# Kernel optimization log

Measured on AMD Instinct MI355X. Metric: run time of the kernel, lower is better.

## Reference

```python
import jax, jax.numpy as jnp
import numpy as np

N, NNODES, CIN, COUT = 64, 512, 32, 64


def setup_inputs() -> dict:
    key = jax.random.key(0)
    k1, k2, k3, k4, k5 = jax.random.split(key, 5)
    A = jax.random.normal(k1, (N, NNODES, NNODES), dtype=jnp.float32)
    X = jax.random.normal(k2, (N, NNODES, CIN), dtype=jnp.float32)
    A_coeffs = jax.random.normal(k3, (5 + 2 * CIN,), dtype=jnp.float32)
    x_num = 4 + 2 * CIN
    scale = np.sqrt(2.0) / (COUT + x_num)
    X_coeffs_1 = jax.random.normal(k4, (COUT, x_num), dtype=jnp.float32) * scale
    X_coeffs_2 = jax.random.normal(k5, (COUT, x_num), dtype=jnp.float32) * scale
    return {"A": A, "X": X, "A_coeffs": A_coeffs,
            "X_coeffs_1": X_coeffs_1, "X_coeffs_2": X_coeffs_2}


def _forward(A, X, A_coeffs, W1, W2):
    n = A.shape[-1]
    C = X.shape[-1]
    Xt = jnp.swapaxes(X, -1, -2)                      # N,C,n
    diag = jnp.diagonal(A, axis1=-2, axis2=-1)        # N,n
    mean_diag = diag.mean(-1)                         # N
    mean_cols = A.mean(-1)                            # N,n
    mean_all = mean_cols.mean(-1)                     # N
    mean_X = Xt.mean(-1)                              # N,C

    c = A_coeffs
    w6 = c[5:5 + C]                                   # coeffs for a6 (X_i + X_j)
    w7 = c[5 + C:5 + 2 * C]                           # coeffs for a7 (mean_X)
    # Fold the 'd,ndij->nij' contraction over the 7 basis tensors into
    # scalar/row/col broadcast terms (identical math, no N x (5+2C) x n x n tensor).
    s = jnp.einsum('c,nci->ni', w6, Xt)               # N,n
    const = c[1] * mean_all + c[2] * mean_diag + jnp.einsum('c,nc->n', w7, mean_X)
    vec = c[3] * mean_cols + c[4] * diag + s          # N,n
    A_t = c[0] * A + const[:, None, None] + vec[:, :, None] + vec[:, None, :]

    # X basis out_x: N x (4+2C) x n, order [x1, x2, x3, x4, x5, x6]
    ones_n = jnp.ones((1, 1, n), A.dtype)
    out_x = jnp.concatenate([
        Xt,                                           # x1: N,C,n
        mean_X[:, :, None] * ones_n,                  # x2: N,C,n
        mean_cols[:, None, :],                        # x3: N,1,n
        diag[:, None, :],                             # x4: N,1,n
        mean_diag[:, None, None] * ones_n,            # x5: N,1,n
        mean_all[:, None, None] * ones_n,             # x6: N,1,n
    ], axis=1)
    X1 = jnp.einsum('bd,ndi->nbi', W1, out_x)         # N,B,n
    X2 = jnp.einsum('bd,ndi->nbi', W2, out_x)         # N,B,n
    out = jnp.einsum('nij,nbj->nbi', A_t, X1) / n + X2  # N,B,n
    return jnp.swapaxes(out, -1, -2)                  # N,n,B


def reference(A, X, A_coeffs, X_coeffs_1, X_coeffs_2):
    return _forward(A, X, A_coeffs, X_coeffs_1, X_coeffs_2)
```

## Files before the change

### kernel.cpp

```cpp
#include <hip/hip_runtime.h>
#include <hip/hip_bf16.h>

#define NB 64
#define NN 512
#define CI 32
#define CO 64
#define XN 68
#define YR 80

typedef __attribute__((ext_vector_type(8))) short bf16x8;
typedef __attribute__((ext_vector_type(4))) float f32x4;

__device__ inline short f2bf(float f) {
  union { __hip_bfloat16 h; unsigned short u; } cv;
  cv.h = __float2bfloat16(f);
  return (short)cv.u;
}

__device__ inline bf16x8 cvt8(float4 a, float4 b) {
  bf16x8 r;
  r[0] = f2bf(a.x); r[1] = f2bf(a.y); r[2] = f2bf(a.z); r[3] = f2bf(a.w);
  r[4] = f2bf(b.x); r[5] = f2bf(b.y); r[6] = f2bf(b.z); r[7] = f2bf(b.w);
  return r;
}

__device__ inline bf16x8 cvt8s(float4 a, float4 b, float s) {
  bf16x8 r;
  r[0] = f2bf(a.x * s); r[1] = f2bf(a.y * s); r[2] = f2bf(a.z * s); r[3] = f2bf(a.w * s);
  r[4] = f2bf(b.x * s); r[5] = f2bf(b.y * s); r[6] = f2bf(b.z * s); r[7] = f2bf(b.w * s);
  return r;
}

__global__ __launch_bounds__(256) void k1x(
    const float* __restrict__ A, const float* __restrict__ X,
    const float* __restrict__ cf, const float* __restrict__ W1,
    float* __restrict__ mc, float* __restrict__ dg, float* __restrict__ vec,
    float* __restrict__ pA, float* __restrict__ pD,
    float* __restrict__ pmX, float* __restrict__ ptC, float* __restrict__ pS,
    unsigned short* __restrict__ Yext) {
  int b = blockIdx.x, ch = blockIdx.y;
  int t = threadIdx.x, w = t >> 6, lane = t & 63;
  int r0 = ch * 16;
  const float* Ab = A + (size_t)b * NN * NN;
  __shared__ float sXc[16][33];
  __shared__ float scf[69];
  __shared__ float sMc[16], sDg[16], sVec[16], wsum[4];

  if (t < 69) scf[t] = cf[t];
  {
    int j = t >> 4, c = (t & 15) * 2;
    float2 xv = *(const float2*)(X + ((size_t)b * NN + r0 + j) * CI + c);
    sXc[j][c] = xv.x; sXc[j][c + 1] = xv.y;
  }
  float4 v0[4], v1[4];
#pragma unroll
  for (int m = 0; m < 4; ++m) {
    const float* rp = Ab + (size_t)(r0 + w * 4 + m) * NN;
    v0[m] = *(const float4*)(rp + lane * 4);
    v1[m] = *(const float4*)(rp + 256 + lane * 4);
  }
  float accR = 0.f;
#pragma unroll
  for (int m = 0; m < 4; ++m) {
    float s = (v0[m].x + v0[m].y) + (v0[m].z + v0[m].w) +
              (v1[m].x + v1[m].y) + (v1[m].z + v1[m].w);
#pragma unroll
    for (int off = 1; off < 64; off <<= 1) s += __shfl_xor(s, off, 64);
    if (lane == 0) {
      float m_ = s * (1.0f / NN);
      mc[b * NN + r0 + w * 4 + m] = m_;
      sMc[w * 4 + m] = m_;
    }
    accR += s;
  }
  if (lane == 0) wsum[w] = accR;
  if (t < 16) {
    float d = Ab[(size_t)(r0 + t) * NN + r0 + t];
    dg[b * NN + r0 + t] = d;
    sDg[t] = d;
  }
  __syncthreads();

  if (t < 16) {
    float u = 0.f;
#pragma unroll
    for (int c = 0; c < CI; ++c) u += scf[5 + c] * sXc[t][c];
    float vj = scf[3] * sMc[t] + scf[4] * sDg[t] + u;
    vec[b * NN + r0 + t] = vj;
    sVec[t] = vj;
  } else if (t == 16) {
    pA[b * 32 + ch] = wsum[0] + wsum[1] + wsum[2] + wsum[3];
    float sd = 0.f;
#pragma unroll
    for (int k = 0; k < 16; ++k) sd += sDg[k];
    pD[b * 32 + ch] = sd;
  }

  {
    int ra = lane & 15, kg = lane >> 4, g = lane >> 4;
    const float* wp = W1 + (w * 16 + ra) * XN + kg * 8;
    bf16x8 wf = cvt8(*(const float4*)wp, *(const float4*)(wp + 4));
    const float* xp = &sXc[ra][kg * 8];
    bf16x8 xf = cvt8(*(const float4*)xp, *(const float4*)(xp + 4));
    f32x4 zero = {0.f, 0.f, 0.f, 0.f};
    f32x4 d = __builtin_amdgcn_mfma_f32_16x16x32_bf16(xf, wf, zero, 0, 0, 0);
    union { unsigned short u[4]; uint2 v; } pk;
#pragma unroll
    for (int r = 0; r < 4; ++r) pk.u[r] = (unsigned short)f2bf(d[r]);
    *(uint2*)(Yext + ((size_t)b * YR + w * 16 + ra) * NN + r0 + g * 4) = pk.v;
  }
  if (t < 16) {
    Yext[((size_t)b * YR + 64) * NN + r0 + t] = (unsigned short)f2bf(sMc[t]);
  } else if (t < 32) {
    Yext[((size_t)b * YR + 65) * NN + r0 + (t - 16)] = (unsigned short)f2bf(sDg[t - 16]);
  } else if (t < 32 + 224) {
    int u2 = t - 32;
    int row = 66 + (u2 >> 4), col = r0 + (u2 & 15);
    Yext[((size_t)b * YR + row) * NN + col] = 0;
  }
  __syncthreads();

  if (t < 32) {
    float s1 = 0.f, s2 = 0.f;
#pragma unroll
    for (int r = 0; r < 16; ++r) {
      float xv = sXc[r][t];
      s1 += xv;
      s2 += sVec[r] * xv;
    }
    pmX[((size_t)b * 32 + ch) * 32 + t] = s1;
    ptC[((size_t)b * 32 + ch) * 32 + t] = s2;
  } else if (t < 35) {
    float s = 0.f;
    if (t == 32) { for (int r = 0; r < 16; ++r) s += sVec[r]; }
    if (t == 33) { for (int r = 0; r < 16; ++r) s += sVec[r] * sMc[r]; }
    if (t == 34) { for (int r = 0; r < 16; ++r) s += sVec[r] * sDg[r]; }
    pS[((size_t)b * 32 + ch) * 3 + (t - 32)] = s;
  }
}

__global__ __launch_bounds__(256) void kW(
    const float* __restrict__ cf, const float* __restrict__ W1,
    const float* __restrict__ W2, const float* __restrict__ pA,
    const float* __restrict__ pD, const float* __restrict__ pmX,
    const float* __restrict__ ptC, const float* __restrict__ pS,
    float* __restrict__ colv, float* __restrict__ sconst) {
  int gb = blockIdx.x, t = threadIdx.x;
  int bb0 = gb * 4;
  __shared__ float sW1[64][69], sW2[64][69];
  __shared__ float mXs[4][33], tCs[4][33];
  __shared__ float scal[4][6];
  __shared__ float scf[69];
  if (t < 69) scf[t] = cf[t];
  for (int idx = t; idx < 64 * XN; idx += 256) {
    int r = idx / XN, c = idx - r * XN;
    sW1[r][c] = W1[idx];
    sW2[r][c] = W2[idx];
  }
  if (t < 128) {
    int bb = t >> 5, c = t & 31, b = bb0 + bb;
    float s1 = 0.f, s2 = 0.f;
#pragma unroll
    for (int k = 0; k < 32; ++k) {
      s1 += pmX[((size_t)b * 32 + k) * 32 + c];
      s2 += ptC[((size_t)b * 32 + k) * 32 + c];
    }
    mXs[bb][c] = s1 * (1.0f / NN);
    tCs[bb][c] = s2;
  } else if (t < 132) {
    int bb = t - 128, b = bb0 + bb;
    float sA = 0.f, sD = 0.f;
#pragma unroll
    for (int k = 0; k < 32; ++k) { sA += pA[b * 32 + k]; sD += pD[b * 32 + k]; }
    scal[bb][0] = sD * (1.0f / NN);
    scal[bb][1] = sA * (1.0f / ((float)NN * (float)NN));
  } else if (t < 136) {
    int bb = t - 132, b = bb0 + bb;
    float s1 = 0.f, s2 = 0.f, s3 = 0.f;
#pragma unroll
    for (int k = 0; k < 32; ++k) {
      s1 += pS[((size_t)b * 32 + k) * 3 + 0];
      s2 += pS[((size_t)b * 32 + k) * 3 + 1];
      s3 += pS[((size_t)b * 32 + k) * 3 + 2];
    }
    scal[bb][2] = s1; scal[bb][3] = s2; scal[bb][4] = s3;
  }
  __syncthreads();
  if (t < 4) {
    float s7 = 0.f;
#pragma unroll
    for (int c = 0; c < CI; ++c) s7 += scf[5 + CI + c] * mXs[t][c];
    sconst[bb0 + t] = scf[1] * scal[t][1] + scf[2] * scal[t][0] + s7;
  }
  {
    int bb = t >> 6, o = t & 63, b = bb0 + bb;
    float w1mX = 0.f, a1 = 0.f, a2 = 0.f, wt = 0.f;
#pragma unroll
    for (int c = 0; c < CI; ++c) {
      float m = mXs[bb][c];
      w1mX += sW1[o][c] * m;
      a1 += sW1[o][CI + c] * m;
      a2 += sW2[o][CI + c] * m;
      wt += sW1[o][c] * tCs[bb][c];
    }
    float smd = scal[bb][0], sma = scal[bb][1];
    a1 += sW1[o][66] * smd + sW1[o][67] * sma;
    a2 += sW2[o][66] * smd + sW2[o][67] * sma;
    float we0 = sW1[o][64], we1 = sW1[o][65];
    float S1n = w1mX + a1 + we0 * sma + we1 * smd;
    float SVn = (wt + a1 * scal[bb][2] + we0 * scal[bb][3] + we1 * scal[bb][4]) * (1.0f / NN);
    float4 cva = make_float4(S1n, a2 + SVn, sW2[o][64] + scf[0] * a1, sW2[o][65]);
    float4 cvb = make_float4(we0, we1, 0.f, 0.f);
    *(float4*)&colv[((size_t)b * CO + o) * 8] = cva;
    *(float4*)&colv[((size_t)b * CO + o) * 8 + 4] = cvb;
  }
}

__global__ __launch_bounds__(256) void k5_mfma(
    const float* __restrict__ A, const unsigned short* __restrict__ Yext,
    const float* __restrict__ X, const float* __restrict__ W2,
    const float* __restrict__ vec, const float* __restrict__ mc,
    const float* __restrict__ dg, const float* __restrict__ colv,
    const float* __restrict__ sconst, const float* __restrict__ cf,
    float* __restrict__ out) {
  int b = blockIdx.x, ic = blockIdx.y;
  int t = threadIdx.x, w = t >> 6, lane = t & 63;
  int ra = lane & 15, kg = lane >> 4, g = lane >> 4;
  int i0 = ic * 64 + w * 16;

  float c0n = cf[0] * (1.0f / NN);
  const float* Arow = A + ((size_t)(b * NN + i0 + ra)) * NN;
  const unsigned short* Yb = Yext + (size_t)b * YR * NN;

  f32x4 acc[4] = {{0.f, 0.f, 0.f, 0.f}, {0.f, 0.f, 0.f, 0.f},
                  {0.f, 0.f, 0.f, 0.f}, {0.f, 0.f, 0.f, 0.f}};
  f32x4 acc4 = {0.f, 0.f, 0.f, 0.f};

#pragma unroll
  for (int jt = 0; jt < 16; ++jt) {
    int kb = jt * 32 + kg * 8;
    float4 a0 = *(const float4*)(Arow + kb);
    float4 a1 = *(const float4*)(Arow + kb + 4);
    bf16x8 af = cvt8s(a0, a1, c0n);
#pragma unroll
    for (int to = 0; to < 4; ++to) {
      bf16x8 bf = *(const bf16x8*)(Yb + (size_t)(to * 16 + ra) * NN + kb);
      acc[to] = __builtin_amdgcn_mfma_f32_16x16x32_bf16(af, bf, acc[to], 0, 0, 0);
    }
    bf16x8 bf4 = *(const bf16x8*)(Yb + (size_t)(64 + ra) * NN + kb);
    acc4 = __builtin_amdgcn_mfma_f32_16x16x32_bf16(af, bf4, acc4, 0, 0, 0);
  }

  {
    const float* xp = X + (size_t)(b * NN + i0 + ra) * CI + kg * 8;
    bf16x8 xf = cvt8(*(const float4*)xp, *(const float4*)(xp + 4));
#pragma unroll
    for (int to = 0; to < 4; ++to) {
      const float* wp = W2 + (size_t)(to * 16 + ra) * XN + kg * 8;
      bf16x8 wf = cvt8(*(const float4*)wp, *(const float4*)(wp + 4));
      acc[to] = __builtin_amdgcn_mfma_f32_16x16x32_bf16(xf, wf, acc[to], 0, 0, 0);
    }
  }

  float Gm[4], Gd[4];
#pragma unroll
  for (int r = 0; r < 4; ++r) {
    Gm[r] = __shfl(acc4[r], lane & 48, 64);
    Gd[r] = __shfl(acc4[r], (lane & 48) | 1, 64);
  }

  float4 v4 = *(const float4*)&vec[b * NN + i0 + g * 4];
  float4 m4 = *(const float4*)&mc[b * NN + i0 + g * 4];
  float4 d4 = *(const float4*)&dg[b * NN + i0 + g * 4];
  float sc = sconst[b];
  float vp[4] = {v4.x + sc, v4.y + sc, v4.z + sc, v4.w + sc};
  float mr[4] = {m4.x, m4.y, m4.z, m4.w};
  float dr[4] = {d4.x, d4.y, d4.z, d4.w};

#pragma unroll
  for (int to = 0; to < 4; ++to) {
    int o = to * 16 + ra;
    float4 cva = *(const float4*)&colv[((size_t)b * CO + o) * 8];
    float4 cvb = *(const float4*)&colv[((size_t)b * CO + o) * 8 + 4];
#pragma unroll
    for (int r = 0; r < 4; ++r) {
      float val = acc[to][r] + vp[r] * cva.x + cva.y + mr[r] * cva.z +
                  dr[r] * cva.w + Gm[r] * cvb.x + Gd[r] * cvb.y;
      out[((size_t)(b * NN + i0 + g * 4 + r)) * CO + o] = val;
    }
  }
}

extern "C" void kernel_launch(void* const* d_in, const int* in_sizes, int n_in,
                              void* d_out, int out_size, void* d_ws, size_t ws_size,
                              hipStream_t stream) {
  const float* A = (const float*)d_in[0];
  const float* X = (const float*)d_in[1];
  const float* cf = (const float*)d_in[2];
  const float* W1 = (const float*)d_in[3];
  const float* W2 = (const float*)d_in[4];
  float* out = (float*)d_out;

  float* p = (float*)d_ws;
  float* mc = p;      p += NB * NN;
  float* dg = p;      p += NB * NN;
  float* vec = p;     p += NB * NN;
  float* pA = p;      p += NB * 32;
  float* pD = p;      p += NB * 32;
  float* pmX = p;     p += NB * 32 * 32;
  float* ptC = p;     p += NB * 32 * 32;
  float* pS = p;      p += NB * 32 * 3;
  float* colv = p;    p += NB * CO * 8;
  float* sconst = p;  p += NB;
  unsigned short* Yext = (unsigned short*)p;

  k1x<<<dim3(NB, 32), 256, 0, stream>>>(A, X, cf, W1, mc, dg, vec,
                                        pA, pD, pmX, ptC, pS, Yext);
  kW<<<16, 256, 0, stream>>>(cf, W1, W2, pA, pD, pmX, ptC, pS, colv, sconst);
  k5_mfma<<<dim3(NB, 8), 256, 0, stream>>>(A, Yext, X, W2, vec, mc, dg,
                                           colv, sconst, cf, out);
}
```

Before: 54.59 us.

## Split k5 reduction across two waves per row group and prescale Y by c0/n

The main A·Y MFMA kernel now uses 512 threads, with two waves splitting the 512-wide K dimension for each 16-row group. Partial accumulators are summed through shared memory before the epilogue. The c0/n scale moves from per-element A conversion in k5 into the Y rows written by k1x, so k5 no longer multiplies every A element. This doubles the waves in flight to hide global-load latency, at the cost of a shared-memory reduction, a barrier, and idle waves during the epilogue. Because the scale is now applied to Y before the bf16 rounding rather than to A, rounding behaviour changes slightly.

```diff
diff --git a/kernel.cpp b/kernel.cpp
--- a/kernel.cpp
+++ b/kernel.cpp
@@ -21,13 +21,6 @@
   bf16x8 r;
   r[0] = f2bf(a.x); r[1] = f2bf(a.y); r[2] = f2bf(a.z); r[3] = f2bf(a.w);
   r[4] = f2bf(b.x); r[5] = f2bf(b.y); r[6] = f2bf(b.z); r[7] = f2bf(b.w);
-  return r;
-}
-
-__device__ inline bf16x8 cvt8s(float4 a, float4 b, float s) {
-  bf16x8 r;
-  r[0] = f2bf(a.x * s); r[1] = f2bf(a.y * s); r[2] = f2bf(a.z * s); r[3] = f2bf(a.w * s);
-  r[4] = f2bf(b.x * s); r[5] = f2bf(b.y * s); r[6] = f2bf(b.z * s); r[7] = f2bf(b.w * s);
   return r;
 }
 
@@ -81,6 +74,8 @@
   }
   __syncthreads();
 
+  float c0n = scf[0] * (1.0f / NN);
+
   if (t < 16) {
     float u = 0.f;
 #pragma unroll
@@ -106,13 +101,13 @@
     f32x4 d = __builtin_amdgcn_mfma_f32_16x16x32_bf16(xf, wf, zero, 0, 0, 0);
     union { unsigned short u[4]; uint2 v; } pk;
 #pragma unroll
-    for (int r = 0; r < 4; ++r) pk.u[r] = (unsigned short)f2bf(d[r]);
+    for (int r = 0; r < 4; ++r) pk.u[r] = (unsigned short)f2bf(d[r] * c0n);
     *(uint2*)(Yext + ((size_t)b * YR + w * 16 + ra) * NN + r0 + g * 4) = pk.v;
   }
   if (t < 16) {
-    Yext[((size_t)b * YR + 64) * NN + r0 + t] = (unsigned short)f2bf(sMc[t]);
+    Yext[((size_t)b * YR + 64) * NN + r0 + t] = (unsigned short)f2bf(sMc[t] * c0n);
   } else if (t < 32) {
-    Yext[((size_t)b * YR + 65) * NN + r0 + (t - 16)] = (unsigned short)f2bf(sDg[t - 16]);
+    Yext[((size_t)b * YR + 65) * NN + r0 + (t - 16)] = (unsigned short)f2bf(sDg[t - 16] * c0n);
   } else if (t < 32 + 224) {
     int u2 = t - 32;
     int row = 66 + (u2 >> 4), col = r0 + (u2 & 15);
@@ -216,19 +211,20 @@
   }
 }
 
-__global__ __launch_bounds__(256) void k5_mfma(
+__global__ __launch_bounds__(512, 4) void k5_mfma(
     const float* __restrict__ A, const unsigned short* __restrict__ Yext,
     const float* __restrict__ X, const float* __restrict__ W2,
     const float* __restrict__ vec, const float* __restrict__ mc,
     const float* __restrict__ dg, const float* __restrict__ colv,
-    const float* __restrict__ sconst, const float* __restrict__ cf,
-    float* __restrict__ out) {
+    const float* __restrict__ sconst, float* __restrict__ out) {
   int b = blockIdx.x, ic = blockIdx.y;
   int t = threadIdx.x, w = t >> 6, lane = t & 63;
+  int rg = w >> 1, q = w & 1;
   int ra = lane & 15, kg = lane >> 4, g = lane >> 4;
-  int i0 = ic * 64 + w * 16;
-
-  float c0n = cf[0] * (1.0f / NN);
+  int i0 = ic * 64 + rg * 16;
+  __shared__ float sAcc[4][16][68];
+  __shared__ float sG4[4][16][2];
+
   const float* Arow = A + ((size_t)(b * NN + i0 + ra)) * NN;
   const unsigned short* Yb = Yext + (size_t)b * YR * NN;
 
@@ -237,11 +233,11 @@
   f32x4 acc4 = {0.f, 0.f, 0.f, 0.f};
 
 #pragma unroll
-  for (int jt = 0; jt < 16; ++jt) {
-    int kb = jt * 32 + kg * 8;
+  for (int jt = 0; jt < 8; ++jt) {
+    int kb = q * 256 + jt * 32 + kg * 8;
     float4 a0 = *(const float4*)(Arow + kb);
     float4 a1 = *(const float4*)(Arow + kb + 4);
-    bf16x8 af = cvt8s(a0, a1, c0n);
+    bf16x8 af = cvt8(a0, a1);
 #pragma unroll
     for (int to = 0; to < 4; ++to) {
       bf16x8 bf = *(const bf16x8*)(Yb + (size_t)(to * 16 + ra) * NN + kb);
@@ -251,42 +247,75 @@
     acc4 = __builtin_amdgcn_mfma_f32_16x16x32_bf16(af, bf4, acc4, 0, 0, 0);
   }
 
-  {
-    const float* xp = X + (size_t)(b * NN + i0 + ra) * CI + kg * 8;
-    bf16x8 xf = cvt8(*(const float4*)xp, *(const float4*)(xp + 4));
+  float4 v4, m4, d4;
+  float sc = 0.f;
+  float4 cva[4], cvb[4];
+  if (q == 1) {
+#pragma unroll
+    for (int to = 0; to < 4; ++to)
+#pragma unroll
+      for (int r = 0; r < 4; ++r)
+        sAcc[rg][g * 4 + r][to * 16 + ra] = acc[to][r];
+    if (ra < 2) {
+#pragma unroll
+      for (int r = 0; r < 4; ++r) sG4[rg][g * 4 + r][ra] = acc4[r];
+    }
+  } else {
+    v4 = *(const float4*)&vec[b * NN + i0 + g * 4];
+    m4 = *(const float4*)&mc[b * NN + i0 + g * 4];
+    d4 = *(const float4*)&dg[b * NN + i0 + g * 4];
+    sc = sconst[b];
 #pragma unroll
     for (int to = 0; to < 4; ++to) {
-      const float* wp = W2 + (size_t)(to * 16 + ra) * XN + kg * 8;
-      bf16x8 wf = cvt8(*(const float4*)wp, *(const float4*)(wp + 4));
-      acc[to] = __builtin_amdgcn_mfma_f32_16x16x32_bf16(xf, wf, acc[to], 0, 0, 0);
-    }
-  }
-
-  float Gm[4], Gd[4];
-#pragma unroll
-  for (int r = 0; r < 4; ++r) {
-    Gm[r] = __shfl(acc4[r], lane & 48, 64);
-    Gd[r] = __shfl(acc4[r], (lane & 48) | 1, 64);
-  }
-
-  float4 v4 = *(const float4*)&vec[b * NN + i0 + g * 4];
-  float4 m4 = *(const float4*)&mc[b * NN + i0 + g * 4];
-  float4 d4 = *(const float4*)&dg[b * NN + i0 + g * 4];
-  float sc = sconst[b];
-  float vp[4] = {v4.x + sc, v4.y + sc, v4.z + sc, v4.w + sc};
-  float mr[4] = {m4.x, m4.y, m4.z, m4.w};
-  float dr[4] = {d4.x, d4.y, d4.z, d4.w};
-
-#pragma unroll
-  for (int to = 0; to < 4; ++to) {
-    int o = to * 16 + ra;
-    float4 cva = *(const float4*)&colv[((size_t)b * CO + o) * 8];
-    float4 cvb = *(const float4*)&colv[((size_t)b * CO + o) * 8 + 4];
+      int o = to * 16 + ra;
+      cva[to] = *(const float4*)&colv[((size_t)b * CO + o) * 8];
+      cvb[to] = *(const float4*)&colv[((size_t)b * CO + o) * 8 + 4];
+    }
+  }
+  __syncthreads();
+
+  if (q == 0) {
+#pragma unroll
+    for (int to = 0; to < 4; ++to)
+#pragma unroll
+      for (int r = 0; r < 4; ++r)
+        acc[to][r] += sAcc[rg][g * 4 + r][to * 16 + ra];
+    if (ra < 2) {
+#pragma unroll
+      for (int r = 0; r < 4; ++r) acc4[r] += sG4[rg][g * 4 + r][ra];
+    }
+
+    {
+      const float* xp = X + (size_t)(b * NN + i0 + ra) * CI + kg * 8;
+      bf16x8 xf = cvt8(*(const float4*)xp, *(const float4*)(xp + 4));
+#pragma unroll
+      for (int to = 0; to < 4; ++to) {
+        const float* wp = W2 + (size_t)(to * 16 + ra) * XN + kg * 8;
+        bf16x8 wf = cvt8(*(const float4*)wp, *(const float4*)(wp + 4));
+        acc[to] = __builtin_amdgcn_mfma_f32_16x16x32_bf16(xf, wf, acc[to], 0, 0, 0);
+      }
+    }
+
+    float Gm[4], Gd[4];
 #pragma unroll
     for (int r = 0; r < 4; ++r) {
-      float val = acc[to][r] + vp[r] * cva.x + cva.y + mr[r] * cva.z +
-                  dr[r] * cva.w + Gm[r] * cvb.x + Gd[r] * cvb.y;
-      out[((size_t)(b * NN + i0 + g * 4 + r)) * CO + o] = val;
+      Gm[r] = __shfl(acc4[r], lane & 48, 64);
+      Gd[r] = __shfl(acc4[r], (lane & 48) | 1, 64);
+    }
+
+    float vp[4] = {v4.x + sc, v4.y + sc, v4.z + sc, v4.w + sc};
+    float mr[4] = {m4.x, m4.y, m4.z, m4.w};
+    float dr[4] = {d4.x, d4.y, d4.z, d4.w};
+
+#pragma unroll
+    for (int to = 0; to < 4; ++to) {
+      int o = to * 16 + ra;
+#pragma unroll
+      for (int r = 0; r < 4; ++r) {
+        float val = acc[to][r] + vp[r] * cva[to].x + cva[to].y + mr[r] * cva[to].z +
+                    dr[r] * cva[to].w + Gm[r] * cvb[to].x + Gd[r] * cvb[to].y;
+        out[((size_t)(b * NN + i0 + g * 4 + r)) * CO + o] = val;
+      }
     }
   }
 }
@@ -317,6 +346,6 @@
   k1x<<<dim3(NB, 32), 256, 0, stream>>>(A, X, cf, W1, mc, dg, vec,
                                         pA, pD, pmX, ptC, pS, Yext);
   kW<<<16, 256, 0, stream>>>(cf, W1, W2, pA, pD, pmX, ptC, pS, colv, sconst);
-  k5_mfma<<<dim3(NB, 8), 256, 0, stream>>>(A, Yext, X, W2, vec, mc, dg,
-                                           colv, sconst, cf, out);
-}
+  k5_mfma<<<dim3(NB, 8), 512, 0, stream>>>(A, Yext, X, W2, vec, mc, dg,
+                                           colv, sconst, out);
+}
```

After: 56.09 us. +2.8%, slower.

## Stage A tiles through double-buffered swizzled LDS and split output columns across waves

Applied to the files above, without the earlier changes.

The main GEMM kernel now uses 512-thread blocks. Each block cooperatively loads 64x64 chunks of A, converts them to bf16 and stores them in double-buffered, XOR-swizzled shared memory, prefetching the next chunk while MFMAs run on the current one. Waves are split into row-group and output-column halves, and the Gm/Gd extras are exchanged through shared memory instead of shuffles. The c0/n scale is folded into Y when k1x writes it, so A no longer needs a per-element multiply, and the grid is reordered so consecutive blocks share a batch. The cost is more block-level synchronisation and more shared memory per block.

```diff
diff --git a/kernel.cpp b/kernel.cpp
--- a/kernel.cpp
+++ b/kernel.cpp
@@ -21,13 +21,6 @@
   bf16x8 r;
   r[0] = f2bf(a.x); r[1] = f2bf(a.y); r[2] = f2bf(a.z); r[3] = f2bf(a.w);
   r[4] = f2bf(b.x); r[5] = f2bf(b.y); r[6] = f2bf(b.z); r[7] = f2bf(b.w);
-  return r;
-}
-
-__device__ inline bf16x8 cvt8s(float4 a, float4 b, float s) {
-  bf16x8 r;
-  r[0] = f2bf(a.x * s); r[1] = f2bf(a.y * s); r[2] = f2bf(a.z * s); r[3] = f2bf(a.w * s);
-  r[4] = f2bf(b.x * s); r[5] = f2bf(b.y * s); r[6] = f2bf(b.z * s); r[7] = f2bf(b.w * s);
   return r;
 }
 
@@ -81,6 +74,8 @@
   }
   __syncthreads();
 
+  float c0n = scf[0] * (1.0f / NN);
+
   if (t < 16) {
     float u = 0.f;
 #pragma unroll
@@ -106,13 +101,13 @@
     f32x4 d = __builtin_amdgcn_mfma_f32_16x16x32_bf16(xf, wf, zero, 0, 0, 0);
     union { unsigned short u[4]; uint2 v; } pk;
 #pragma unroll
-    for (int r = 0; r < 4; ++r) pk.u[r] = (unsigned short)f2bf(d[r]);
+    for (int r = 0; r < 4; ++r) pk.u[r] = (unsigned short)f2bf(d[r] * c0n);
     *(uint2*)(Yext + ((size_t)b * YR + w * 16 + ra) * NN + r0 + g * 4) = pk.v;
   }
   if (t < 16) {
-    Yext[((size_t)b * YR + 64) * NN + r0 + t] = (unsigned short)f2bf(sMc[t]);
+    Yext[((size_t)b * YR + 64) * NN + r0 + t] = (unsigned short)f2bf(sMc[t] * c0n);
   } else if (t < 32) {
-    Yext[((size_t)b * YR + 65) * NN + r0 + (t - 16)] = (unsigned short)f2bf(sDg[t - 16]);
+    Yext[((size_t)b * YR + 65) * NN + r0 + (t - 16)] = (unsigned short)f2bf(sDg[t - 16] * c0n);
   } else if (t < 32 + 224) {
     int u2 = t - 32;
     int row = 66 + (u2 >> 4), col = r0 + (u2 & 15);
@@ -216,77 +211,112 @@
   }
 }
 
-__global__ __launch_bounds__(256) void k5_mfma(
+__global__ __launch_bounds__(512, 4) void k5_mfma(
     const float* __restrict__ A, const unsigned short* __restrict__ Yext,
     const float* __restrict__ X, const float* __restrict__ W2,
     const float* __restrict__ vec, const float* __restrict__ mc,
     const float* __restrict__ dg, const float* __restrict__ colv,
-    const float* __restrict__ sconst, const float* __restrict__ cf,
-    float* __restrict__ out) {
-  int b = blockIdx.x, ic = blockIdx.y;
+    const float* __restrict__ sconst, float* __restrict__ out) {
+  int ic = blockIdx.x, b = blockIdx.y;
   int t = threadIdx.x, w = t >> 6, lane = t & 63;
+  int rg = w >> 1, oc = w & 1;
   int ra = lane & 15, kg = lane >> 4, g = lane >> 4;
-  int i0 = ic * 64 + w * 16;
-
-  float c0n = cf[0] * (1.0f / NN);
-  const float* Arow = A + ((size_t)(b * NN + i0 + ra)) * NN;
+  int i0 = ic * 64;
+  int wr0 = rg * 16;
+  __shared__ unsigned short sA[2][64 * 64];
+  __shared__ float sGm[64], sGd[64];
+
   const unsigned short* Yb = Yext + (size_t)b * YR * NN;
 
-  f32x4 acc[4] = {{0.f, 0.f, 0.f, 0.f}, {0.f, 0.f, 0.f, 0.f},
-                  {0.f, 0.f, 0.f, 0.f}, {0.f, 0.f, 0.f, 0.f}};
+  int st_r = t >> 3, st_k = t & 7;
+  const float* Agl = A + ((size_t)(b * NN + i0 + st_r)) * NN + st_k * 8;
+  int st_addr = st_r * 64 + ((st_k ^ (st_r & 7)) << 3);
+
+  {
+    float4 a0 = *(const float4*)(Agl);
+    float4 a1 = *(const float4*)(Agl + 4);
+    *(bf16x8*)&sA[0][st_addr] = cvt8(a0, a1);
+  }
+  __syncthreads();
+
+  f32x4 acc[2] = {{0.f, 0.f, 0.f, 0.f}, {0.f, 0.f, 0.f, 0.f}};
   f32x4 acc4 = {0.f, 0.f, 0.f, 0.f};
-
-#pragma unroll
-  for (int jt = 0; jt < 16; ++jt) {
-    int kb = jt * 32 + kg * 8;
-    float4 a0 = *(const float4*)(Arow + kb);
-    float4 a1 = *(const float4*)(Arow + kb + 4);
-    bf16x8 af = cvt8s(a0, a1, c0n);
-#pragma unroll
-    for (int to = 0; to < 4; ++to) {
-      bf16x8 bf = *(const bf16x8*)(Yb + (size_t)(to * 16 + ra) * NN + kb);
-      acc[to] = __builtin_amdgcn_mfma_f32_16x16x32_bf16(af, bf, acc[to], 0, 0, 0);
-    }
-    bf16x8 bf4 = *(const bf16x8*)(Yb + (size_t)(64 + ra) * NN + kb);
-    acc4 = __builtin_amdgcn_mfma_f32_16x16x32_bf16(af, bf4, acc4, 0, 0, 0);
-  }
-
-  {
-    const float* xp = X + (size_t)(b * NN + i0 + ra) * CI + kg * 8;
+  int arow = wr0 + ra;
+  int abase = arow * 64;
+  int aswz = arow & 7;
+
+  for (int c = 0; c < 8; ++c) {
+    int cur = c & 1;
+    float4 na0, na1;
+    if (c < 7) {
+      na0 = *(const float4*)(Agl + (c + 1) * 64);
+      na1 = *(const float4*)(Agl + (c + 1) * 64 + 4);
+    }
+#pragma unroll
+    for (int kb = 0; kb < 2; ++kb) {
+      bf16x8 af = *(const bf16x8*)&sA[cur][abase + (((kb * 4 + kg) ^ aswz) << 3)];
+      int kcol = c * 64 + kb * 32 + kg * 8;
+#pragma unroll
+      for (int to = 0; to < 2; ++to) {
+        bf16x8 bf = *(const bf16x8*)(Yb + (size_t)(oc * 32 + to * 16 + ra) * NN + kcol);
+        acc[to] = __builtin_amdgcn_mfma_f32_16x16x32_bf16(af, bf, acc[to], 0, 0, 0);
+      }
+      if (oc == 0) {
+        bf16x8 bf4 = *(const bf16x8*)(Yb + (size_t)(64 + ra) * NN + kcol);
+        acc4 = __builtin_amdgcn_mfma_f32_16x16x32_bf16(af, bf4, acc4, 0, 0, 0);
+      }
+    }
+    if (c < 7) {
+      *(bf16x8*)&sA[cur ^ 1][st_addr] = cvt8(na0, na1);
+    }
+    __syncthreads();
+  }
+
+  {
+    const float* xp = X + (size_t)(b * NN + i0 + wr0 + ra) * CI + kg * 8;
     bf16x8 xf = cvt8(*(const float4*)xp, *(const float4*)(xp + 4));
 #pragma unroll
-    for (int to = 0; to < 4; ++to) {
-      const float* wp = W2 + (size_t)(to * 16 + ra) * XN + kg * 8;
+    for (int to = 0; to < 2; ++to) {
+      const float* wp = W2 + (size_t)(oc * 32 + to * 16 + ra) * XN + kg * 8;
       bf16x8 wf = cvt8(*(const float4*)wp, *(const float4*)(wp + 4));
       acc[to] = __builtin_amdgcn_mfma_f32_16x16x32_bf16(xf, wf, acc[to], 0, 0, 0);
     }
   }
 
-  float Gm[4], Gd[4];
-#pragma unroll
-  for (int r = 0; r < 4; ++r) {
-    Gm[r] = __shfl(acc4[r], lane & 48, 64);
-    Gd[r] = __shfl(acc4[r], (lane & 48) | 1, 64);
-  }
-
-  float4 v4 = *(const float4*)&vec[b * NN + i0 + g * 4];
-  float4 m4 = *(const float4*)&mc[b * NN + i0 + g * 4];
-  float4 d4 = *(const float4*)&dg[b * NN + i0 + g * 4];
+  if (oc == 0 && ra < 2) {
+#pragma unroll
+    for (int r = 0; r < 4; ++r) {
+      if (ra == 0) sGm[wr0 + g * 4 + r] = acc4[r];
+      else         sGd[wr0 + g * 4 + r] = acc4[r];
+    }
+  }
+  __syncthreads();
+
+  float4 v4 = *(const float4*)&vec[b * NN + i0 + wr0 + g * 4];
+  float4 m4 = *(const float4*)&mc[b * NN + i0 + wr0 + g * 4];
+  float4 d4 = *(const float4*)&dg[b * NN + i0 + wr0 + g * 4];
   float sc = sconst[b];
   float vp[4] = {v4.x + sc, v4.y + sc, v4.z + sc, v4.w + sc};
   float mr[4] = {m4.x, m4.y, m4.z, m4.w};
   float dr[4] = {d4.x, d4.y, d4.z, d4.w};
-
-#pragma unroll
-  for (int to = 0; to < 4; ++to) {
-    int o = to * 16 + ra;
+  float Gm[4], Gd[4];
+#pragma unroll
+  for (int r = 0; r < 4; ++r) {
+    int row = wr0 + g * 4 + r;
+    Gm[r] = sGm[row];
+    Gd[r] = sGd[row];
+  }
+
+#pragma unroll
+  for (int to = 0; to < 2; ++to) {
+    int o = oc * 32 + to * 16 + ra;
     float4 cva = *(const float4*)&colv[((size_t)b * CO + o) * 8];
     float4 cvb = *(const float4*)&colv[((size_t)b * CO + o) * 8 + 4];
 #pragma unroll
     for (int r = 0; r < 4; ++r) {
       float val = acc[to][r] + vp[r] * cva.x + cva.y + mr[r] * cva.z +
                   dr[r] * cva.w + Gm[r] * cvb.x + Gd[r] * cvb.y;
-      out[((size_t)(b * NN + i0 + g * 4 + r)) * CO + o] = val;
+      out[((size_t)(b * NN + i0 + wr0 + g * 4 + r)) * CO + o] = val;
     }
   }
 }
@@ -317,6 +347,6 @@
   k1x<<<dim3(NB, 32), 256, 0, stream>>>(A, X, cf, W1, mc, dg, vec,
                                         pA, pD, pmX, ptC, pS, Yext);
   kW<<<16, 256, 0, stream>>>(cf, W1, W2, pA, pD, pmX, ptC, pS, colv, sconst);
-  k5_mfma<<<dim3(NB, 8), 256, 0, stream>>>(A, Yext, X, W2, vec, mc, dg,
-                                           colv, sconst, cf, out);
-}
+  k5_mfma<<<dim3(8, NB), 512, 0, stream>>>(A, Yext, X, W2, vec, mc, dg,
+                                           colv, sconst, out);
+}
```

Result: no change. 54.58 us (-0.0%).
